# Kernel tuning notes

Hardware: AMD Instinct MI355X
Metric: run time of the kernel (lower is better)

The kernel has to match this reference:

```python
import jax, jax.numpy as jnp
import numpy as np

B, N, QD, H, D = 2, 2048, 1152, 16, 72
INNER = H * D
RETAIN_RATE = 0.4  # layer_count in [4, 64] branch
N_KEEP = int(N * RETAIN_RATE)
N_PRUNE = N - N_KEEP
SCALE = D ** (-0.5)


def setup_inputs() -> dict:
    key = jax.random.key(0)
    ks = jax.random.split(key, 6)
    s = 0.02
    return {
        "x": jax.random.normal(ks[0], (B, N, QD), jnp.float32),
        "Wq": jax.random.normal(ks[1], (QD, INNER), jnp.float32) * s,
        "Wk": jax.random.normal(ks[2], (QD, INNER), jnp.float32) * s,
        "Wv": jax.random.normal(ks[3], (QD, INNER), jnp.float32) * s,
        "Wo": jax.random.normal(ks[4], (INNER, QD), jnp.float32) * s,
        "bo": jnp.zeros((QD,), jnp.float32),
    }


def reference(x, Wq, Wk, Wv, Wo, bo):
    b = x.shape[0]
    # self-attention: context = x
    q = (x @ Wq).reshape(b, N, H, D).transpose(0, 2, 1, 3)  # [b,H,N,D]
    k = (x @ Wk).reshape(b, N, H, D).transpose(0, 2, 1, 3)
    v = (x @ Wv).reshape(b, N, H, D).transpose(0, 2, 1, 3)

    # ---- WPR pruning pass: full attention map, mean over heads ----
    logits = jnp.einsum('bhnd,bhmd->bhnm', q, k) * SCALE  # [b,H,N,N]
    M = jax.nn.softmax(logits, axis=-1)
    attn = M.mean(axis=1)  # [b,N,N]

    # 5-step power iteration: dist = (1/N) @ attn^5
    dist = jnp.full((b, 1, N), 1.0 / N, dtype=attn.dtype)
    for _ in range(5):
        dist = dist @ attn
    importance = dist[:, 0]  # [b,N]

    _, imp_inds = jax.lax.top_k(importance, N_KEEP)
    _, prune_inds = jax.lax.top_k(-importance, N_PRUNE)
    # boolean-mask selection in torch returns rows in ascending index order
    sorted_imp = jnp.sort(imp_inds, axis=1)      # [b,N_KEEP]
    sorted_prune = jnp.sort(prune_inds, axis=1)  # [b,N_PRUNE]

    selected_rows = jnp.take_along_axis(attn, sorted_imp[:, :, None], axis=1)  # [b,N_KEEP,N]
    max_inds = jnp.argmax(selected_rows, axis=1)  # [b,N]: most-attending retained row per token
    sim_inds = jnp.take_along_axis(max_inds, sorted_prune, axis=1)  # [b,N_PRUNE]

    # ---- attention among retained tokens only ----
    gi = sorted_imp[:, None, :, None]  # broadcast gather index
    q_r = jnp.take_along_axis(q, gi, axis=2)  # [b,H,N_KEEP,D]
    k_r = jnp.take_along_axis(k, gi, axis=2)
    v_r = jnp.take_along_axis(v, gi, axis=2)
    attn_r = jax.nn.softmax(jnp.einsum('bhnd,bhmd->bhnm', q_r, k_r) * SCALE, axis=-1)
    out_r = jnp.einsum('bhnm,bhmd->bhnd', attn_r, v_r)  # [b,H,N_KEEP,D]
    out_r = out_r.transpose(0, 2, 1, 3).reshape(b, N_KEEP, INNER)

    # similarity-based recovery for pruned tokens
    out_p = jnp.take_along_axis(out_r, sim_inds[:, :, None], axis=1)  # [b,N_PRUNE,INNER]

    bidx = jnp.arange(b)[:, None]
    out = jnp.zeros((b, N, INNER), out_r.dtype)
    out = out.at[bidx, sorted_imp].set(out_r)
    out = out.at[bidx, sorted_prune].set(out_p)

    return out @ Wo + bo
```

## Files before the change

kernel.cpp:

```cpp
#include <hip/hip_runtime.h>

namespace {
constexpr int B = 2;
constexpr int N = 2048;
constexpr int QD = 1152;
constexpr int H = 16;
constexpr int D = 72;
constexpr int INNER = 1152;
constexpr int NKEEP = 819;
constexpr int PSL = 32;
constexpr int ILEN = N / PSL;
constexpr int DP = 80;
constexpr int LSTR = 88;
constexpr int ASL = 8;
constexpr int ACH = (NKEEP + ASL - 1) / ASL;
}

#define FINF __builtin_inff()
#define SCALE 0.11785113019775793f

typedef __attribute__((ext_vector_type(8))) __bf16 bf16x8;
typedef __attribute__((ext_vector_type(16))) float f32x16;
typedef __attribute__((ext_vector_type(8))) short short8;

__device__ __forceinline__ f32x16 mfma_bf16(bf16x8 a, bf16x8 b, f32x16 c) {
  return __builtin_amdgcn_mfma_f32_32x32x16_bf16(a, b, c, 0, 0, 0);
}
__device__ __forceinline__ short f2bf(float x) {
  unsigned u = __float_as_uint(x);
  unsigned r = (u + 0x7fffu + ((u >> 16) & 1u)) >> 16;
  return (short)r;
}
__device__ __forceinline__ float bf2f(short b) {
  return __uint_as_float(((unsigned)(unsigned short)b) << 16);
}

__global__ __launch_bounds__(256) void k_xsplit(
    const float* __restrict__ X, short* __restrict__ Xh, short* __restrict__ Xl,
    int total)
{
  int g = blockIdx.x * 256 + threadIdx.x;
  if (g >= total) return;
  float v = X[g];
  short hb = f2bf(v);
  Xh[g] = hb;
  Xl[g] = f2bf(v - bf2f(hb));
}

__global__ __launch_bounds__(256) void k_wsplit3(
    const float* __restrict__ W0, const float* __restrict__ W1,
    const float* __restrict__ W2, short* __restrict__ WTh, short* __restrict__ WTl)
{
  __shared__ float tile[64][65];
  const int tid = threadIdx.x;
  const int k0 = blockIdx.y * 64, n0 = blockIdx.x * 64;
  const int z = blockIdx.z;
  const float* W = (z == 0) ? W0 : (z == 1) ? W1 : W2;
  const size_t zoff = (size_t)z * QD * INNER;
  {
    int r = tid >> 2, c0 = (tid & 3) * 16;
#pragma unroll
    for (int j = 0; j < 16; j += 4) {
      float4 v = *(const float4*)&W[(size_t)(k0 + r) * 1152 + n0 + c0 + j];
      tile[r][c0 + j] = v.x; tile[r][c0 + j + 1] = v.y;
      tile[r][c0 + j + 2] = v.z; tile[r][c0 + j + 3] = v.w;
    }
  }
  __syncthreads();
  for (int e = tid; e < 4096; e += 256) {
    int nr = e >> 6, kc = e & 63;
    float v = tile[kc][nr];
    short hb = f2bf(v);
    WTh[zoff + (size_t)(n0 + nr) * 1152 + k0 + kc] = hb;
    WTl[zoff + (size_t)(n0 + nr) * 1152 + k0 + kc] = f2bf(v - bf2f(hb));
  }
}

__global__ __launch_bounds__(256) void k_wsplitT(
    const float* __restrict__ W, short* __restrict__ WTh, short* __restrict__ WTl)
{
  __shared__ float tile[64][65];
  const int tid = threadIdx.x;
  const int k0 = blockIdx.y * 64, n0 = blockIdx.x * 64;
  {
    int r = tid >> 2, c0 = (tid & 3) * 16;
#pragma unroll
    for (int j = 0; j < 16; j += 4) {
      float4 v = *(const float4*)&W[(size_t)(k0 + r) * 1152 + n0 + c0 + j];
      tile[r][c0 + j] = v.x; tile[r][c0 + j + 1] = v.y;
      tile[r][c0 + j + 2] = v.z; tile[r][c0 + j + 3] = v.w;
    }
  }
  __syncthreads();
  for (int e = tid; e < 4096; e += 256) {
    int nr = e >> 6, kc = e & 63;
    float v = tile[kc][nr];
    short hb = f2bf(v);
    WTh[(size_t)(n0 + nr) * 1152 + k0 + kc] = hb;
    WTl[(size_t)(n0 + nr) * 1152 + k0 + kc] = f2bf(v - bf2f(hb));
  }
}

__global__ __launch_bounds__(256, 2) void k_pgemm3(
    const short* __restrict__ Ah_g, const short* __restrict__ Al_g,
    const short* __restrict__ Bh_g, const short* __restrict__ Bl_g,
    short* __restrict__ QKV0)
{
  constexpr int LK = 40;
  __shared__ short AhS[128 * LK], AlS[128 * LK], BhS[128 * LK], BlS[128 * LK];
  const int tid = threadIdx.x;
  const int wv = tid >> 6, ln = tid & 63;
  const int col = ln & 31, hi = ln >> 5;
  const int wm = wv >> 1, wn = wv & 1;
  const int m0 = blockIdx.y * 128, n0 = blockIdx.x * 128;
  f32x16 acc[2][2];
#pragma unroll
  for (int mi = 0; mi < 2; ++mi)
#pragma unroll
    for (int ni = 0; ni < 2; ++ni)
#pragma unroll
      for (int r = 0; r < 16; ++r) acc[mi][ni][r] = 0.f;

  for (int kt = 0; kt < 1152; kt += 32) {
    __syncthreads();
    for (int e = tid; e < 512; e += 256) {
      int r = e >> 2, c4 = e & 3;
      size_t sa = (size_t)(m0 + r) * 1152 + kt + c4 * 8;
      *(float4*)&AhS[r * LK + c4 * 8] = *(const float4*)(Ah_g + sa);
      *(float4*)&AlS[r * LK + c4 * 8] = *(const float4*)(Al_g + sa);
      size_t sb = (size_t)(n0 + r) * 1152 + kt + c4 * 8;
      *(float4*)&BhS[r * LK + c4 * 8] = *(const float4*)(Bh_g + sb);
      *(float4*)&BlS[r * LK + c4 * 8] = *(const float4*)(Bl_g + sb);
    }
    __syncthreads();
#pragma unroll
    for (int kc = 0; kc < 2; ++kc) {
      bf16x8 ah[2], al[2], bh[2], bl[2];
#pragma unroll
      for (int mi = 0; mi < 2; ++mi) {
        int r = wm * 64 + mi * 32 + col;
        ah[mi] = *(const bf16x8*)&AhS[r * LK + kc * 16 + hi * 8];
        al[mi] = *(const bf16x8*)&AlS[r * LK + kc * 16 + hi * 8];
      }
#pragma unroll
      for (int ni = 0; ni < 2; ++ni) {
        int r = wn * 64 + ni * 32 + col;
        bh[ni] = *(const bf16x8*)&BhS[r * LK + kc * 16 + hi * 8];
        bl[ni] = *(const bf16x8*)&BlS[r * LK + kc * 16 + hi * 8];
      }
#pragma unroll
      for (int mi = 0; mi < 2; ++mi)
#pragma unroll
        for (int ni = 0; ni < 2; ++ni) {
          acc[mi][ni] = mfma_bf16(ah[mi], bh[ni], acc[mi][ni]);
          acc[mi][ni] = mfma_bf16(ah[mi], bl[ni], acc[mi][ni]);
          acc[mi][ni] = mfma_bf16(al[mi], bh[ni], acc[mi][ni]);
        }
    }
  }
  const size_t S = (size_t)65536 * 80;
#pragma unroll
  for (int mi = 0; mi < 2; ++mi)
#pragma unroll
    for (int ni = 0; ni < 2; ++ni)
#pragma unroll
      for (int r = 0; r < 16; ++r) {
        int m = m0 + wm * 64 + mi * 32 + (r & 3) + 8 * (r >> 2) + 4 * hi;
        int c = n0 + wn * 64 + ni * 32 + col;
        int which = c / 1152, cm = c - which * 1152;
        int hh = cm / 72, dd = cm - hh * 72;
        int b = m >> 11, nn = m & 2047;
        size_t idx = (((size_t)(b * 16 + hh)) * 2048 + nn) * 80 + dd;
        float v = acc[mi][ni][r];
        short hb = f2bf(v);
        short* OH = QKV0 + (size_t)which * 2 * S;
        OH[idx] = hb;
        OH[S + idx] = f2bf(v - bf2f(hb));
      }
}

__global__ __launch_bounds__(256, 2) void k_stats3(
    const short* __restrict__ Qh, const short* __restrict__ Ql,
    const short* __restrict__ Kh, const short* __restrict__ Kl,
    float* __restrict__ inv_out)
{
  __shared__ __align__(16) short kh[64 * LSTR];
  __shared__ __align__(16) short kl[64 * LSTR];
  const int tid = threadIdx.x;
  const int wv = tid >> 6, ln = tid & 63;
  const int col = ln & 31, hi = ln >> 5;
  const int q0 = blockIdx.x * 256;
  const int h = blockIdx.y, b = blockIdx.z;
  const size_t bhbase = (size_t)(b * H + h) * N * DP;

  bf16x8 qfh[2][5], qfl[2][5];
#pragma unroll
  for (int mi = 0; mi < 2; ++mi) {
    const size_t rb = bhbase + (size_t)(q0 + wv * 64 + mi * 32 + col) * DP + hi * 8;
#pragma unroll
    for (int d = 0; d < 5; ++d) {
      qfh[mi][d] = *(const bf16x8*)(const void*)(Qh + rb + d * 16);
      qfl[mi][d] = *(const bf16x8*)(const void*)(Ql + rb + d * 16);
    }
  }
  float s[2][16];
#pragma unroll
  for (int mi = 0; mi < 2; ++mi)
#pragma unroll
    for (int r = 0; r < 16; ++r) s[mi][r] = 0.f;

  float4 rkh[3], rkl[3];
  auto LOADK = [&](int kt) {
#pragma unroll
    for (int ss = 0; ss < 3; ++ss) {
      int e = ss * 256 + tid;
      if (e < 640) {
        int r = e / 10, cc = e - r * 10;
        size_t sb = bhbase + (size_t)(kt + r) * DP + cc * 8;
        rkh[ss] = *(const float4*)(const void*)(Kh + sb);
        rkl[ss] = *(const float4*)(const void*)(Kl + sb);
      }
    }
  };
  auto STOREK = [&]() {
#pragma unroll
    for (int ss = 0; ss < 3; ++ss) {
      int e = ss * 256 + tid;
      if (e < 640) {
        int r = e / 10, cc = e - r * 10;
        *(float4*)(void*)(kh + r * LSTR + cc * 8) = rkh[ss];
        *(float4*)(void*)(kl + r * LSTR + cc * 8) = rkl[ss];
      }
    }
  };

  LOADK(0);
  for (int kt = 0; kt < N; kt += 64) {
    __syncthreads();
    STOREK();
    __syncthreads();
    if (kt + 64 < N) LOADK(kt + 64);
    f32x16 z[2][2];
#pragma unroll
    for (int mi = 0; mi < 2; ++mi)
#pragma unroll
      for (int rn = 0; rn < 2; ++rn)
#pragma unroll
        for (int r = 0; r < 16; ++r) z[mi][rn][r] = 0.f;
#pragma unroll
    for (int d = 0; d < 5; ++d) {
      const int boff = d * 16 + hi * 8;
      bf16x8 bh0 = *(const bf16x8*)(const void*)(kh + col * LSTR + boff);
      bf16x8 bl0 = *(const bf16x8*)(const void*)(kl + col * LSTR + boff);
      bf16x8 bh1 = *(const bf16x8*)(const void*)(kh + (32 + col) * LSTR + boff);
      bf16x8 bl1 = *(const bf16x8*)(const void*)(kl + (32 + col) * LSTR + boff);
#pragma unroll
      for (int mi = 0; mi < 2; ++mi) {
        z[mi][0] = mfma_bf16(qfh[mi][d], bh0, z[mi][0]);
        z[mi][0] = mfma_bf16(qfh[mi][d], bl0, z[mi][0]);
        z[mi][0] = mfma_bf16(qfl[mi][d], bh0, z[mi][0]);
        z[mi][1] = mfma_bf16(qfh[mi][d], bh1, z[mi][1]);
        z[mi][1] = mfma_bf16(qfh[mi][d], bl1, z[mi][1]);
        z[mi][1] = mfma_bf16(qfl[mi][d], bh1, z[mi][1]);
      }
    }
#pragma unroll
    for (int mi = 0; mi < 2; ++mi)
#pragma unroll
      for (int r = 0; r < 16; ++r)
        s[mi][r] += __expf(z[mi][0][r] * SCALE) + __expf(z[mi][1][r] * SCALE);
  }
#pragma unroll
  for (int mi = 0; mi < 2; ++mi)
#pragma unroll
    for (int r = 0; r < 16; ++r) {
      float v = s[mi][r];
#pragma unroll
      for (int o = 1; o < 32; o <<= 1) v += __shfl_xor(v, o);
      if (col == 0) {
        int row = q0 + wv * 64 + mi * 32 + ((r & 3) + ((r >> 2) << 3) + (hi << 2));
        inv_out[(size_t)(b * H + h) * N + row] = 1.0f / v;
      }
    }
}

__global__ __launch_bounds__(256, 2) void k_attn3(
    const short* __restrict__ Qh, const short* __restrict__ Ql,
    const short* __restrict__ Kh, const short* __restrict__ Kl,
    const float* __restrict__ inv_in, float* __restrict__ attn)
{
  __shared__ __align__(16) short kh[64 * LSTR];
  __shared__ __align__(16) short kl[64 * LSTR];
  __shared__ float invs[256];
  const int tid = threadIdx.x;
  const int wv = tid >> 6, ln = tid & 63;
  const int col = ln & 31, hi = ln >> 5;
  const int k0 = blockIdx.x * 64, q0 = blockIdx.y * 256, b = blockIdx.z;

  f32x16 pa[2][2];
#pragma unroll
  for (int mi = 0; mi < 2; ++mi)
#pragma unroll
    for (int rn = 0; rn < 2; ++rn)
#pragma unroll
      for (int r = 0; r < 16; ++r) pa[mi][rn][r] = 0.f;

  float4 rkh[3], rkl[3];
  float rin;
  auto LOADH = [&](int h) {
    const size_t hb = (size_t)(b * H + h) * N * DP;
#pragma unroll
    for (int ss = 0; ss < 3; ++ss) {
      int e = ss * 256 + tid;
      if (e < 640) {
        int r = e / 10, cc = e - r * 10;
        size_t sb = hb + (size_t)(k0 + r) * DP + cc * 8;
        rkh[ss] = *(const float4*)(const void*)(Kh + sb);
        rkl[ss] = *(const float4*)(const void*)(Kl + sb);
      }
    }
    rin = inv_in[(size_t)(b * H + h) * N + q0 + tid];
  };
  auto STOREH = [&]() {
#pragma unroll
    for (int ss = 0; ss < 3; ++ss) {
      int e = ss * 256 + tid;
      if (e < 640) {
        int r = e / 10, cc = e - r * 10;
        *(float4*)(void*)(kh + r * LSTR + cc * 8) = rkh[ss];
        *(float4*)(void*)(kl + r * LSTR + cc * 8) = rkl[ss];
      }
    }
    invs[tid] = rin;
  };

  LOADH(0);
  for (int h = 0; h < H; ++h) {
    __syncthreads();
    STOREH();
    __syncthreads();
    if (h + 1 < H) LOADH(h + 1);

    const size_t bhbase = (size_t)(b * H + h) * N * DP;
    f32x16 z[2][2];
#pragma unroll
    for (int mi = 0; mi < 2; ++mi)
#pragma unroll
      for (int rn = 0; rn < 2; ++rn)
#pragma unroll
        for (int r = 0; r < 16; ++r) z[mi][rn][r] = 0.f;

#pragma unroll
    for (int d = 0; d < 5; ++d) {
      const int boff = d * 16 + hi * 8;
      bf16x8 bh0 = *(const bf16x8*)(const void*)(kh + col * LSTR + boff);
      bf16x8 bl0 = *(const bf16x8*)(const void*)(kl + col * LSTR + boff);
      bf16x8 bh1 = *(const bf16x8*)(const void*)(kh + (32 + col) * LSTR + boff);
      bf16x8 bl1 = *(const bf16x8*)(const void*)(kl + (32 + col) * LSTR + boff);
      bf16x8 qh0 = *(const bf16x8*)(const void*)(Qh + bhbase + (size_t)(q0 + wv * 64 + col) * DP + boff);
      bf16x8 ql0 = *(const bf16x8*)(const void*)(Ql + bhbase + (size_t)(q0 + wv * 64 + col) * DP + boff);
      bf16x8 qh1 = *(const bf16x8*)(const void*)(Qh + bhbase + (size_t)(q0 + wv * 64 + 32 + col) * DP + boff);
      bf16x8 ql1 = *(const bf16x8*)(const void*)(Ql + bhbase + (size_t)(q0 + wv * 64 + 32 + col) * DP + boff);
      z[0][0] = mfma_bf16(qh0, bh0, z[0][0]);
      z[0][0] = mfma_bf16(qh0, bl0, z[0][0]);
      z[0][0] = mfma_bf16(ql0, bh0, z[0][0]);
      z[0][1] = mfma_bf16(qh0, bh1, z[0][1]);
      z[0][1] = mfma_bf16(qh0, bl1, z[0][1]);
      z[0][1] = mfma_bf16(ql0, bh1, z[0][1]);
      z[1][0] = mfma_bf16(qh1, bh0, z[1][0]);
      z[1][0] = mfma_bf16(qh1, bl0, z[1][0]);
      z[1][0] = mfma_bf16(ql1, bh0, z[1][0]);
      z[1][1] = mfma_bf16(qh1, bh1, z[1][1]);
      z[1][1] = mfma_bf16(qh1, bl1, z[1][1]);
      z[1][1] = mfma_bf16(ql1, bh1, z[1][1]);
    }
#pragma unroll
    for (int mi = 0; mi < 2; ++mi)
#pragma unroll
      for (int r = 0; r < 16; ++r) {
        const int rloc = wv * 64 + mi * 32 + (r & 3) + ((r >> 2) << 3) + (hi << 2);
        const float iv = invs[rloc];
        pa[mi][0][r] += __expf(z[mi][0][r] * SCALE) * iv;
        pa[mi][1][r] += __expf(z[mi][1][r] * SCALE) * iv;
      }
  }
  const float invH = 1.0f / H;
#pragma unroll
  for (int mi = 0; mi < 2; ++mi)
#pragma unroll
    for (int r = 0; r < 16; ++r) {
      const int row = q0 + wv * 64 + mi * 32 + (r & 3) + ((r >> 2) << 3) + (hi << 2);
      attn[((size_t)b * N + row) * N + k0 + col] = pa[mi][0][r] * invH;
      attn[((size_t)b * N + row) * N + k0 + 32 + col] = pa[mi][1][r] * invH;
    }
}

__global__ __launch_bounds__(256) void k_power(
    const float* __restrict__ attn, float* __restrict__ partial)
{
  int g = blockIdx.x * 256 + threadIdx.x;
  int sy = blockIdx.y;
  int b = g / N, j = g % N;
  const float* ab = attn + (size_t)b * N * N;
  int i0 = sy * ILEN;
  float sum = 0.f;
  for (int i = i0; i < i0 + ILEN; ++i) sum += ab[(size_t)i * N + j];
  partial[(size_t)sy * (B * N) + g] = sum * (1.0f / N);
}

__global__ __launch_bounds__(256) void k_powfused(
    const float* __restrict__ attn, const float* __restrict__ partial_in,
    float* __restrict__ partial_out)
{
  __shared__ float red[4][64];
  __shared__ float ds[64];
  const int tid = threadIdx.x;
  const int g = blockIdx.x * 256 + tid;
  const int sy = blockIdx.y;
  const int b = g / N, j = g % N;
  const int i0 = sy * ILEN;
  {
    int i = tid & 63, sgrp = tid >> 6;
    const float* p = partial_in + (size_t)(b * N + i0 + i);
    float s8 = 0.f;
#pragma unroll
    for (int k = 0; k < 8; ++k) s8 += p[(size_t)(sgrp * 8 + k) * (B * N)];
    red[sgrp][i] = s8;
  }
  __syncthreads();
  if (tid < 64) ds[tid] = red[0][tid] + red[1][tid] + red[2][tid] + red[3][tid];
  __syncthreads();
  const float* ab = attn + (size_t)b * N * N;
  float sum = 0.f;
  for (int i = 0; i < ILEN; ++i) sum += ds[i] * ab[(size_t)(i0 + i) * N + j];
  partial_out[(size_t)sy * (B * N) + g] = sum;
}

__global__ __launch_bounds__(256) void k_powred(
    const float* __restrict__ partial, float* __restrict__ dout)
{
  int g = blockIdx.x * 256 + threadIdx.x;
  if (g >= B * N) return;
  float s = 0.f;
  for (int sy = 0; sy < PSL; ++sy) s += partial[(size_t)sy * (B * N) + g];
  dout[g] = s;
}

__global__ __launch_bounds__(1024) void k_partition(
    const float* __restrict__ imp, int* __restrict__ sorted_imp,
    int* __restrict__ keepflag, int* __restrict__ s_map)
{
  __shared__ float v[N];
  __shared__ int   id[N];
  __shared__ int   kf[N];
  __shared__ int   ps[N];
  const int tid = threadIdx.x;
  const int b = blockIdx.x;
  for (int i = tid; i < N; i += 1024) { v[i] = imp[b * N + i]; id[i] = i; }
  for (int k = 2; k <= N; k <<= 1) {
    for (int j = k >> 1; j > 0; j >>= 1) {
      __syncthreads();
      for (int i = tid; i < N; i += 1024) {
        int ixj = i ^ j;
        if (ixj > i) {
          bool up = ((i & k) == 0);
          float va = v[i], vb = v[ixj];
          int ia = id[i], ib = id[ixj];
          bool b_before_a = (vb > va) || (vb == va && ib < ia);
          if (b_before_a == up) { v[i] = vb; v[ixj] = va; id[i] = ib; id[ixj] = ia; }
        }
      }
    }
  }
  __syncthreads();
  for (int i = tid; i < N; i += 1024) kf[id[i]] = (i < NKEEP) ? 1 : 0;
  __syncthreads();
  for (int i = tid; i < N; i += 1024) ps[i] = kf[i];
  for (int off = 1; off < N; off <<= 1) {
    __syncthreads();
    int t0 = (tid >= off) ? ps[tid - off] : 0;
    int i1 = tid + 1024;
    int t1 = ps[i1 - off];
    __syncthreads();
    ps[tid] += t0;
    ps[i1] += t1;
  }
  __syncthreads();
  for (int i = tid; i < N; i += 1024) {
    int excl = ps[i] - kf[i];
    keepflag[b * N + i] = kf[i];
    if (kf[i]) { sorted_imp[b * NKEEP + excl] = i; s_map[b * N + i] = excl; }
  }
}

__global__ __launch_bounds__(256) void k_argmax_part(
    const float* __restrict__ attn, const int* __restrict__ sorted_imp,
    float* __restrict__ pval, int* __restrict__ pidx)
{
  __shared__ int imp_s[ACH];
  const int tid = threadIdx.x;
  const int g = blockIdx.x * 256 + tid;
  const int s = blockIdx.y;
  const int b = g / N, n = g % N;
  const int k0 = s * ACH;
  const int k1 = (k0 + ACH < NKEEP) ? k0 + ACH : NKEEP;
  const int cnt = k1 - k0;
  for (int i = tid; i < cnt; i += 256) imp_s[i] = sorted_imp[b * NKEEP + k0 + i];
  __syncthreads();
  const float* ab = attn + (size_t)b * N * N;
  float best = -FINF; int bi = k0;
  for (int k = 0; k < cnt; ++k) {
    float val = ab[(size_t)imp_s[k] * N + n];
    if (val > best) { best = val; bi = k0 + k; }
  }
  pval[(size_t)s * (B * N) + g] = best;
  pidx[(size_t)s * (B * N) + g] = bi;
}

__global__ __launch_bounds__(256) void k_argmax_comb(
    const float* __restrict__ pval, const int* __restrict__ pidx,
    const int* __restrict__ keepflag, int* __restrict__ s_map)
{
  int g = blockIdx.x * 256 + threadIdx.x;
  if (g >= B * N) return;
  float best = -FINF; int bi = 0;
#pragma unroll
  for (int s = 0; s < ASL; ++s) {
    float v = pval[(size_t)s * (B * N) + g];
    if (v > best) { best = v; bi = pidx[(size_t)s * (B * N) + g]; }
  }
  if (!keepflag[g]) s_map[g] = bi;
}

__global__ __launch_bounds__(256, 2) void k_rfused(
    const short* __restrict__ Qh, const short* __restrict__ Ql,
    const short* __restrict__ Kh, const short* __restrict__ Kl,
    const short* __restrict__ Vh, const int* __restrict__ sorted_imp,
    short* __restrict__ Yh, short* __restrict__ Yl)
{
  constexpr int LK = 88;
  constexpr int VTS = 72;
  __shared__ __align__(16) short KhS[64 * LK];
  __shared__ __align__(16) short KlS[64 * LK];
  __shared__ __align__(16) short VhS[64 * LK];
  __shared__ __align__(16) short VT[72 * VTS];
  __shared__ int imp[NKEEP];
  const int tid = threadIdx.x;
  const int wv = tid >> 6, ln = tid & 63;
  const int col = ln & 31, hi = ln >> 5;
  const int b = blockIdx.z, h = blockIdx.y, q0 = blockIdx.x * 128;
  const size_t bh80 = (size_t)(b * H + h) * N * DP;
  for (int i = tid; i < NKEEP; i += 256) imp[i] = sorted_imp[b * NKEEP + i];
  __syncthreads();
  int qr = q0 + wv * 32 + col;
  int qi = imp[qr < NKEEP ? qr : NKEEP - 1];
  bf16x8 qfh[5], qfl[5];
  {
    const size_t qb = bh80 + (size_t)qi * DP + hi * 8;
#pragma unroll
    for (int d = 0; d < 5; ++d) {
      qfh[d] = *(const bf16x8*)(const void*)(Qh + qb + d * 16);
      qfl[d] = *(const bf16x8*)(const void*)(Ql + qb + d * 16);
    }
  }
  float denom = 0.f;
  f32x16 oacc[3];
#pragma unroll
  for (int nc = 0; nc < 3; ++nc)
#pragma unroll
    for (int r = 0; r < 16; ++r) oacc[nc][r] = 0.f;

  for (int kt = 0; kt < 832; kt += 64) {
    for (int e = tid; e < 640; e += 256) {
      int r = e / 10, cc = e - r * 10;
      int kv = kt + r;
      float4 vkh, vkl, vvh;
      if (kv < NKEEP) {
        size_t sb = bh80 + (size_t)imp[kv] * DP + cc * 8;
        vkh = *(const float4*)(const void*)(Kh + sb);
        vkl = *(const float4*)(const void*)(Kl + sb);
        vvh = *(const float4*)(const void*)(Vh + sb);
      } else {
        vkh = make_float4(0.f, 0.f, 0.f, 0.f); vkl = vkh; vvh = vkh;
      }
      *(float4*)(void*)&KhS[r * LK + cc * 8] = vkh;
      *(float4*)(void*)&KlS[r * LK + cc * 8] = vkl;
      *(float4*)(void*)&VhS[r * LK + cc * 8] = vvh;
    }
    __syncthreads();
    f32x16 z[2];
#pragma unroll
    for (int rn = 0; rn < 2; ++rn)
#pragma unroll
      for (int r = 0; r < 16; ++r) z[rn][r] = 0.f;
#pragma unroll
    for (int d = 0; d < 5; ++d) {
      const int boff = d * 16 + hi * 8;
#pragma unroll
      for (int rn = 0; rn < 2; ++rn) {
        bf16x8 kfh = *(const bf16x8*)(const void*)(KhS + (rn * 32 + col) * LK + boff);
        bf16x8 kfl = *(const bf16x8*)(const void*)(KlS + (rn * 32 + col) * LK + boff);
        z[rn] = mfma_bf16(kfh, qfh[d], z[rn]);
        z[rn] = mfma_bf16(kfh, qfl[d], z[rn]);
        z[rn] = mfma_bf16(kfl, qfh[d], z[rn]);
      }
    }
    for (int e = tid; e < 576; e += 256) {
      int dd = e % 72, k8 = e / 72;
      short8 t;
#pragma unroll
      for (int j = 0; j < 8; ++j) t[j] = VhS[(k8 * 8 + j) * LK + dd];
      *(short8*)(void*)&VT[dd * VTS + k8 * 8] = t;
    }
    const bool full = (kt + 64 <= NKEEP);
#pragma unroll
    for (int rn = 0; rn < 2; ++rn) {
      int kvb = kt + rn * 32 + 4 * hi;
#pragma unroll
      for (int r = 0; r < 16; ++r) {
        float pe = __expf(z[rn][r] * SCALE);
        if (!full) {
          int kv = kvb + (r & 3) + 8 * (r >> 2);
          pe = (kv < NKEEP) ? pe : 0.f;
        }
        z[rn][r] = pe;
        denom += pe;
      }
    }
    __syncthreads();
#pragma unroll
    for (int rn = 0; rn < 2; ++rn) {
#pragma unroll
      for (int kc = 0; kc < 2; ++kc) {
        unsigned p0, p1, p2, p3;
        asm("v_cvt_pk_bf16_f32 %0, %1, %2" : "=v"(p0) : "v"(z[rn][8 * kc + 0]), "v"(z[rn][8 * kc + 1]));
        asm("v_cvt_pk_bf16_f32 %0, %1, %2" : "=v"(p1) : "v"(z[rn][8 * kc + 2]), "v"(z[rn][8 * kc + 3]));
        asm("v_cvt_pk_bf16_f32 %0, %1, %2" : "=v"(p2) : "v"(z[rn][8 * kc + 4]), "v"(z[rn][8 * kc + 5]));
        asm("v_cvt_pk_bf16_f32 %0, %1, %2" : "=v"(p3) : "v"(z[rn][8 * kc + 6]), "v"(z[rn][8 * kc + 7]));
        unsigned othA = hi ? p0 : p2, othB = hi ? p1 : p3;
        unsigned swA = (unsigned)__shfl_xor((int)othA, 32);
        unsigned swB = (unsigned)__shfl_xor((int)othB, 32);
        union { unsigned u[4]; bf16x8 v; } pf;
        pf.u[0] = hi ? swA : p0; pf.u[1] = hi ? swB : p1;
        pf.u[2] = hi ? p2 : swA; pf.u[3] = hi ? p3 : swB;
        const int kb = rn * 32 + kc * 16 + hi * 8;
#pragma unroll
        for (int nc = 0; nc < 3; ++nc) {
          int dr = nc * 32 + col; if (dr > 71) dr = 71;
          bf16x8 vf = *(const bf16x8*)(const void*)(VT + dr * VTS + kb);
          oacc[nc] = mfma_bf16(pf.v, vf, oacc[nc]);
        }
      }
    }
  }
  denom += __shfl_xor(denom, 32);
  float invd = 1.0f / denom;
#pragma unroll
  for (int r = 0; r < 16; ++r) {
    int cr = (r & 3) + 8 * (r >> 2) + 4 * hi;
    int q = q0 + wv * 32 + cr;
    float dv = __shfl(invd, cr);
    if (q < NKEEP) {
#pragma unroll
      for (int nc = 0; nc < 3; ++nc) {
        int dd = nc * 32 + col;
        if (dd < 72) {
          float v = oacc[nc][r] * dv;
          size_t idx = ((size_t)b * NKEEP + q) * 1152 + h * 72 + dd;
          short hb = f2bf(v);
          Yh[idx] = hb;
          Yl[idx] = f2bf(v - bf2f(hb));
        }
      }
    }
  }
}

__global__ __launch_bounds__(256, 2) void k_ogemm(
    const short* __restrict__ Ah_g, const short* __restrict__ Al_g,
    const short* __restrict__ Bh_g, const short* __restrict__ Bl_g,
    float* __restrict__ OutF, const float* __restrict__ bias,
    int Mtot)
{
  constexpr int LK = 40;
  __shared__ short AhS[64 * LK], AlS[64 * LK], BhS[64 * LK], BlS[64 * LK];
  const int tid = threadIdx.x;
  const int wv = tid >> 6, ln = tid & 63;
  const int col = ln & 31, hi = ln >> 5;
  const int wm = wv >> 1, wn = wv & 1;
  const int m0 = blockIdx.y * 64, n0 = blockIdx.x * 64;
  f32x16 acc;
#pragma unroll
  for (int r = 0; r < 16; ++r) acc[r] = 0.f;

  for (int kt = 0; kt < 1152; kt += 32) {
    __syncthreads();
    {
      int e = tid;
      int r = e >> 2, c4 = e & 3;
      int ra = m0 + r; if (ra >= Mtot) ra = Mtot - 1;
      size_t sa = (size_t)ra * 1152 + kt + c4 * 8;
      *(float4*)&AhS[r * LK + c4 * 8] = *(const float4*)(Ah_g + sa);
      *(float4*)&AlS[r * LK + c4 * 8] = *(const float4*)(Al_g + sa);
      size_t sb = (size_t)(n0 + r) * 1152 + kt + c4 * 8;
      *(float4*)&BhS[r * LK + c4 * 8] = *(const float4*)(Bh_g + sb);
      *(float4*)&BlS[r * LK + c4 * 8] = *(const float4*)(Bl_g + sb);
    }
    __syncthreads();
#pragma unroll
    for (int kc = 0; kc < 2; ++kc) {
      int ra = wm * 32 + col;
      int rb = wn * 32 + col;
      bf16x8 ah = *(const bf16x8*)&AhS[ra * LK + kc * 16 + hi * 8];
      bf16x8 al = *(const bf16x8*)&AlS[ra * LK + kc * 16 + hi * 8];
      bf16x8 bh = *(const bf16x8*)&BhS[rb * LK + kc * 16 + hi * 8];
      bf16x8 bl = *(const bf16x8*)&BlS[rb * LK + kc * 16 + hi * 8];
      acc = mfma_bf16(ah, bh, acc);
      acc = mfma_bf16(ah, bl, acc);
      acc = mfma_bf16(al, bh, acc);
    }
  }
#pragma unroll
  for (int r = 0; r < 16; ++r) {
    int m = m0 + wm * 32 + (r & 3) + 8 * (r >> 2) + 4 * hi;
    int c = n0 + wn * 32 + col;
    if (m < Mtot) OutF[(size_t)m * 1152 + c] = acc[r] + bias[c];
  }
}

__global__ __launch_bounds__(256) void k_scatter(
    const float* __restrict__ Y, const int* __restrict__ s_map,
    float* __restrict__ out)
{
  size_t g = (size_t)blockIdx.x * 256 + threadIdx.x;
  if (g >= (size_t)B * N * QD) return;
  int c = (int)(g % QD);
  int n_ = (int)((g / QD) % N);
  int b = (int)(g / ((size_t)N * QD));
  int src = s_map[b * N + n_];
  out[g] = Y[((size_t)b * NKEEP + src) * QD + c];
}

extern "C" void kernel_launch(void* const* d_in, const int* in_sizes, int n_in,
                              void* d_out, int out_size, void* d_ws, size_t ws_size,
                              hipStream_t stream)
{
  const float* x  = (const float*)d_in[0];
  const float* Wq = (const float*)d_in[1];
  const float* Wk = (const float*)d_in[2];
  const float* Wv = (const float*)d_in[3];
  const float* Wo = (const float*)d_in[4];
  const float* bo = (const float*)d_in[5];
  float* out = (float*)d_out;

  char* ws = (char*)d_ws;
  size_t off = 0;
  auto alloc = [&](size_t bytes) -> void* {
    void* p = ws + off;
    off = (off + bytes + 255) & ~(size_t)255;
    return p;
  };
  const int ROWS = B * H * N;
  const size_t XEL = (size_t)B * N * QD;
  const size_t WEL = (size_t)QD * INNER;
  short* xh   = (short*)alloc(sizeof(short) * XEL);
  short* xl   = (short*)alloc(sizeof(short) * XEL);
  short* WTh  = (short*)alloc(sizeof(short) * WEL * 3);
  short* WTl  = (short*)alloc(sizeof(short) * WEL * 3);
  short* Qhb  = (short*)alloc(sizeof(short) * (size_t)ROWS * DP);
  short* Qlb  = (short*)alloc(sizeof(short) * (size_t)ROWS * DP);
  short* Khb  = (short*)alloc(sizeof(short) * (size_t)ROWS * DP);
  short* Klb  = (short*)alloc(sizeof(short) * (size_t)ROWS * DP);
  short* Vhb  = (short*)alloc(sizeof(short) * (size_t)ROWS * DP);
  short* Vlb  = (short*)alloc(sizeof(short) * (size_t)ROWS * DP);
  float* attn = (float*)alloc(sizeof(float) * (size_t)B * N * N);
  float* inv  = (float*)alloc(sizeof(float) * (size_t)ROWS);
  float* dvec = (float*)alloc(sizeof(float) * B * N);
  float* partA = (float*)alloc(sizeof(float) * PSL * B * N);
  float* partB = (float*)alloc(sizeof(float) * PSL * B * N);
  int* sorted_imp = (int*)alloc(sizeof(int) * B * NKEEP);
  int* keepflag   = (int*)alloc(sizeof(int) * B * N);
  int* s_map      = (int*)alloc(sizeof(int) * B * N);
  float* pval     = (float*)alloc(sizeof(float) * ASL * B * N);
  int*   pidx     = (int*)alloc(sizeof(int) * ASL * B * N);
  (void)Vlb;
  short* Yh = xh;
  short* Yl = xh + (size_t)B * NKEEP * INNER;
  float* Y  = (float*)xl;

  dim3 blk(256);

  k_xsplit<<<dim3(((int)XEL + 255) / 256), blk, 0, stream>>>(x, xh, xl, (int)XEL);
  k_wsplit3<<<dim3(QD / 64, QD / 64, 3), blk, 0, stream>>>(Wq, Wk, Wv, WTh, WTl);

  hipMemsetAsync(Qhb, 0, sizeof(short) * (size_t)ROWS * DP * 6, stream);

  k_pgemm3<<<dim3(3 * INNER / 128, (B * N) / 128), blk, 0, stream>>>(
      xh, xl, WTh, WTl, Qhb);

  k_wsplitT<<<dim3(QD / 64, QD / 64), blk, 0, stream>>>(Wo, WTh, WTl);

  k_stats3<<<dim3(N / 256, H, B), blk, 0, stream>>>(Qhb, Qlb, Khb, Klb, inv);
  k_attn3<<<dim3(N / 64, N / 256, B), blk, 0, stream>>>(Qhb, Qlb, Khb, Klb, inv, attn);

  k_power<<<dim3(B * N / 256, PSL), blk, 0, stream>>>(attn, partA);
  k_powfused<<<dim3(B * N / 256, PSL), blk, 0, stream>>>(attn, partA, partB);
  k_powfused<<<dim3(B * N / 256, PSL), blk, 0, stream>>>(attn, partB, partA);
  k_powfused<<<dim3(B * N / 256, PSL), blk, 0, stream>>>(attn, partA, partB);
  k_powfused<<<dim3(B * N / 256, PSL), blk, 0, stream>>>(attn, partB, partA);
  k_powred<<<dim3(B * N / 256), blk, 0, stream>>>(partA, dvec);

  k_partition<<<dim3(B), dim3(1024), 0, stream>>>(dvec, sorted_imp, keepflag, s_map);
  k_argmax_part<<<dim3(B * N / 256, ASL), blk, 0, stream>>>(attn, sorted_imp, pval, pidx);
  k_argmax_comb<<<dim3(B * N / 256), blk, 0, stream>>>(pval, pidx, keepflag, s_map);

  k_rfused<<<dim3((NKEEP + 127) / 128, H, B), blk, 0, stream>>>(
      Qhb, Qlb, Khb, Klb, Vhb, sorted_imp, Yh, Yl);

  k_ogemm<<<dim3(QD / 64, (B * NKEEP + 63) / 64), blk, 0, stream>>>(
      Yh, Yl, WTh, WTl, Y, bo, B * NKEEP);
  k_scatter<<<dim3((int)(((size_t)B * N * QD + 255) / 256)), blk, 0, stream>>>(Y, s_map, out);
}
```

Before: 562.3 us.

## Prefetch next K tile into registers and swizzle block order in QKV GEMM

The QKV projection GEMM now loads the next K-slice from global memory into registers while the MFMAs for the current slice run, then stores it to shared memory after a barrier. This hides global load latency behind compute. Blocks are remapped through a 1D grid swizzle, grouping tiles so neighbouring blocks share A/B rows for L2 reuse. Wo's split copy moves to its own buffer so it can be prepared before the GEMM, at the cost of extra registers and workspace.

```diff
diff --git a/kernel.cpp b/kernel.cpp
--- a/kernel.cpp
+++ b/kernel.cpp
@@ -112,7 +112,34 @@
   const int wv = tid >> 6, ln = tid & 63;
   const int col = ln & 31, hi = ln >> 5;
   const int wm = wv >> 1, wn = wv & 1;
-  const int m0 = blockIdx.y * 128, n0 = blockIdx.x * 128;
+  const int swz = (blockIdx.x & 7) * 108 + (blockIdx.x >> 3);
+  const int m0 = (swz / 27) * 128, n0 = (swz % 27) * 128;
+  const int sr = tid >> 2, sc = (tid & 3) * 8;
+  float4 rah[2], ral[2], rbh[2], rbl[2];
+
+  auto LOAD = [&](int kt) {
+#pragma unroll
+    for (int s = 0; s < 2; ++s) {
+      int r = sr + s * 64;
+      size_t sa = (size_t)(m0 + r) * 1152 + kt + sc;
+      rah[s] = *(const float4*)(const void*)(Ah_g + sa);
+      ral[s] = *(const float4*)(const void*)(Al_g + sa);
+      size_t sb = (size_t)(n0 + r) * 1152 + kt + sc;
+      rbh[s] = *(const float4*)(const void*)(Bh_g + sb);
+      rbl[s] = *(const float4*)(const void*)(Bl_g + sb);
+    }
+  };
+  auto STORE = [&]() {
+#pragma unroll
+    for (int s = 0; s < 2; ++s) {
+      int r = sr + s * 64;
+      *(float4*)(void*)&AhS[r * LK + sc] = rah[s];
+      *(float4*)(void*)&AlS[r * LK + sc] = ral[s];
+      *(float4*)(void*)&BhS[r * LK + sc] = rbh[s];
+      *(float4*)(void*)&BlS[r * LK + sc] = rbl[s];
+    }
+  };
+
   f32x16 acc[2][2];
 #pragma unroll
   for (int mi = 0; mi < 2; ++mi)
@@ -121,18 +148,11 @@
 #pragma unroll
       for (int r = 0; r < 16; ++r) acc[mi][ni][r] = 0.f;
 
+  LOAD(0);
+  STORE();
   for (int kt = 0; kt < 1152; kt += 32) {
     __syncthreads();
-    for (int e = tid; e < 512; e += 256) {
-      int r = e >> 2, c4 = e & 3;
-      size_t sa = (size_t)(m0 + r) * 1152 + kt + c4 * 8;
-      *(float4*)&AhS[r * LK + c4 * 8] = *(const float4*)(Ah_g + sa);
-      *(float4*)&AlS[r * LK + c4 * 8] = *(const float4*)(Al_g + sa);
-      size_t sb = (size_t)(n0 + r) * 1152 + kt + c4 * 8;
-      *(float4*)&BhS[r * LK + c4 * 8] = *(const float4*)(Bh_g + sb);
-      *(float4*)&BlS[r * LK + c4 * 8] = *(const float4*)(Bl_g + sb);
-    }
-    __syncthreads();
+    if (kt + 32 < 1152) LOAD(kt + 32);
 #pragma unroll
     for (int kc = 0; kc < 2; ++kc) {
       bf16x8 ah[2], al[2], bh[2], bl[2];
@@ -157,6 +177,8 @@
           acc[mi][ni] = mfma_bf16(al[mi], bh[ni], acc[mi][ni]);
         }
     }
+    __syncthreads();
+    if (kt + 32 < 1152) STORE();
   }
   const size_t S = (size_t)65536 * 80;
 #pragma unroll
@@ -767,6 +789,8 @@
   short* xl   = (short*)alloc(sizeof(short) * XEL);
   short* WTh  = (short*)alloc(sizeof(short) * WEL * 3);
   short* WTl  = (short*)alloc(sizeof(short) * WEL * 3);
+  short* WoTh = (short*)alloc(sizeof(short) * WEL);
+  short* WoTl = (short*)alloc(sizeof(short) * WEL);
   short* Qhb  = (short*)alloc(sizeof(short) * (size_t)ROWS * DP);
   short* Qlb  = (short*)alloc(sizeof(short) * (size_t)ROWS * DP);
   short* Khb  = (short*)alloc(sizeof(short) * (size_t)ROWS * DP);
@@ -792,13 +816,11 @@
 
   k_xsplit<<<dim3(((int)XEL + 255) / 256), blk, 0, stream>>>(x, xh, xl, (int)XEL);
   k_wsplit3<<<dim3(QD / 64, QD / 64, 3), blk, 0, stream>>>(Wq, Wk, Wv, WTh, WTl);
+  k_wsplitT<<<dim3(QD / 64, QD / 64), blk, 0, stream>>>(Wo, WoTh, WoTl);
 
   hipMemsetAsync(Qhb, 0, sizeof(short) * (size_t)ROWS * DP * 6, stream);
 
-  k_pgemm3<<<dim3(3 * INNER / 128, (B * N) / 128), blk, 0, stream>>>(
-      xh, xl, WTh, WTl, Qhb);
-
-  k_wsplitT<<<dim3(QD / 64, QD / 64), blk, 0, stream>>>(Wo, WTh, WTl);
+  k_pgemm3<<<dim3(864), blk, 0, stream>>>(xh, xl, WTh, WTl, Qhb);
 
   k_stats3<<<dim3(N / 256, H, B), blk, 0, stream>>>(Qhb, Qlb, Khb, Klb, inv);
   k_attn3<<<dim3(N / 64, N / 256, B), blk, 0, stream>>>(Qhb, Qlb, Khb, Klb, inv, attn);
@@ -818,6 +840,6 @@
       Qhb, Qlb, Khb, Klb, Vhb, sorted_imp, Yh, Yl);
 
   k_ogemm<<<dim3(QD / 64, (B * NKEEP + 63) / 64), blk, 0, stream>>>(
-      Yh, Yl, WTh, WTl, Y, bo, B * NKEEP);
+      Yh, Yl, WoTh, WoTl, Y, bo, B * NKEEP);
   k_scatter<<<dim3((int)(((size_t)B * N * QD + 255) / 256)), blk, 0, stream>>>(Y, s_map, out);
 }
```

New measurement: 867.4 us. +54.3%, slower.
